# Performance work log

Measured on AMD Instinct MI355X. Metric: run time of the kernel, lower is better.

Reference implementation:

```python
import jax, jax.numpy as jnp
import numpy as np

HIDDEN = 64
IN_SIZE = 2048 + 512  # sum(obs_shape) + sum(action_shape)


def setup_inputs() -> dict:
    key = jax.random.key(0)
    ks = jax.random.split(key, 10)
    B = 32768
    s_in = 1.0 / np.sqrt(IN_SIZE)
    s_h = 1.0 / np.sqrt(HIDDEN)
    return {
        "state": jax.random.normal(ks[0], (B, 2048), dtype=jnp.float32),
        "action": jax.random.normal(ks[1], (B, 512), dtype=jnp.float32),
        "hidden_state": jax.random.normal(ks[2], (B, HIDDEN), dtype=jnp.float32),
        "cell_state": jax.random.normal(ks[3], (B, HIDDEN), dtype=jnp.float32),
        # fused gate weights, gate order: [i, f, g, o]
        "Wi": jax.random.uniform(ks[4], (IN_SIZE, 4 * HIDDEN), jnp.float32, -s_in, s_in),
        "bi": jax.random.uniform(ks[5], (4 * HIDDEN,), jnp.float32, -s_in, s_in),
        "Wh": jax.random.uniform(ks[6], (HIDDEN, 4 * HIDDEN), jnp.float32, -s_h, s_h),
        "bh": jax.random.uniform(ks[7], (4 * HIDDEN,), jnp.float32, -s_h, s_h),
        "Wo": jax.random.uniform(ks[8], (HIDDEN, 1), jnp.float32, -s_h, s_h),
        "bo": jax.random.uniform(ks[9], (1,), jnp.float32, -s_h, s_h),
    }


def reference(state, action, hidden_state, cell_state, Wi, bi, Wh, bh, Wo, bo):
    x = jnp.concatenate([state, action], axis=1)  # [B, IN_SIZE]
    # two fused GEMMs covering all 8 Linear layers (gate order i,f,g,o)
    gates = x @ Wi + bi + hidden_state @ Wh + bh  # [B, 4*HIDDEN]
    i_t, f_t, g_t, o_t = jnp.split(gates, 4, axis=1)
    i_t = jax.nn.sigmoid(i_t)
    f_t = jax.nn.sigmoid(f_t)
    g_t = jnp.tanh(g_t)
    o_t = jax.nn.sigmoid(o_t)
    c_t = f_t * cell_state + i_t * g_t
    h_t = o_t * jnp.tanh(c_t)
    out = jnp.tanh(h_t @ Wo + bo)  # [B, 1]
    return (out, h_t, c_t)
```

## Files before the change

### kernel.cpp

```cpp
#include <hip/hip_runtime.h>
#include <hip/hip_bf16.h>

#define K_IN 2624
#define NSTEP 82
#define NCHUNK 82

typedef __attribute__((ext_vector_type(8))) short short8;
typedef __attribute__((ext_vector_type(4))) float float4_t;

__device__ __forceinline__ short f2bf(float f) {
    union { __hip_bfloat16 b; short s; } u;
    u.b = __float2bfloat16(f);
    return u.s;
}

__device__ __forceinline__ float sigmoid_fast(float x) {
    return 1.f / (1.f + __expf(-x));
}

__device__ __forceinline__ float tanh_fast(float x) {
    float e = __expf(-2.f * fabsf(x));
    float t = (1.f - e) / (1.f + e);
    return copysignf(t, x);
}

__device__ __forceinline__ void async16(const void* g, void* l) {
    __builtin_amdgcn_global_load_lds(
        (__attribute__((address_space(1))) void*)g,
        (__attribute__((address_space(3))) void*)l, 16, 0, 0);
}

__global__ void prep_kernel(const float* __restrict__ Wi, const float* __restrict__ bi,
                            const float* __restrict__ Wh, const float* __restrict__ bh,
                            short* __restrict__ Wt2, float* __restrict__ bsum) {
    __shared__ short tile[32][264];
    const int t = threadIdx.x;
    const int kb = blockIdx.x;
    const int k0 = kb * 32;

#pragma unroll 8
    for (int j = 0; j < 32; ++j) {
        int k = k0 + j;
        float v = (k < 2560) ? Wi[(size_t)k * 256 + t]
                             : Wh[(size_t)(k - 2560) * 256 + t];
        tile[j][t] = f2bf(v);
    }
    if (kb == 0) bsum[t] = bi[t] + bh[t];
    __syncthreads();

#pragma unroll
    for (int c = 0; c < 4; ++c) {
        int idx = c * 256 + t;
        int lane = idx & 63;
        int nb = idx >> 6;
        int n = nb * 16 + (lane & 15);
        int j0 = (lane >> 4) * 8;
        short8 v;
#pragma unroll
        for (int j = 0; j < 8; ++j) v[j] = tile[j0 + j][n];
        *reinterpret_cast<short8*>(Wt2 + (size_t)kb * 8192 + (size_t)idx * 8) = v;
    }
}

__global__ __launch_bounds__(256, 2)
void lstm_kernel(const float* __restrict__ state, const float* __restrict__ action,
                 const float* __restrict__ hidden, const float* __restrict__ cell,
                 const short* __restrict__ Wt2, const float* __restrict__ bsum,
                 const float* __restrict__ Wo, const float* __restrict__ bo,
                 float* __restrict__ out, int Brows) {
    __shared__ __align__(16) char smem[49152];
    char* const sA = smem;
    char* const sB = smem + 16384;

    const int t = threadIdx.x;
    const int w = t >> 6;
    const int l = t & 63;
    const int lr = l & 15;
    const int q = l >> 4;
    const int bm = blockIdx.x;

    const int rsub = l >> 3;
    const int scol = (l & 7) ^ rsub;
    const char* aSrc[2];
    auto setA = [&](const float* p, int strideF) {
#pragma unroll
        for (int i = 0; i < 2; ++i) {
            size_t grow = (size_t)bm * 64 + w * 16 + i * 8 + rsub;
            aSrc[i] = (const char*)(p + grow * (size_t)strideF) + scol * 16;
        }
    };

    auto issueAB = [&](int buf, const char* bS) {
#pragma unroll
        for (int j = 0; j < 4; ++j)
            async16(bS + j * 1024, sB + buf * 16384 + (w * 4 + j) * 1024);
#pragma unroll
        for (int i = 0; i < 2; ++i) {
            async16(aSrc[i], sA + buf * 8192 + (w * 16 + i * 8) * 128);
            aSrc[i] += 128;
        }
    };

    float4_t acc[16];
#pragma unroll
    for (int nb = 0; nb < 16; ++nb) acc[nb] = (float4_t)(bsum[nb * 16 + lr]);

    setA(state, 2048);
    const char* bS0 = (const char*)Wt2 + (w * 4) * 1024 + l * 16;
    issueAB(0, bS0);
    issueAB(1, bS0 + 16384);
    const char* bSn = bS0 + 2 * 16384;

    const char* const sAb = sA + (w * 16 + lr) * 128;
    const char* const sBb = sB + l * 16;
    const int g0 = (2 * q) ^ (lr & 7);
    const int g1 = (2 * q + 1) ^ (lr & 7);

    auto compute = [&](int buf) {
        const char* bufA = sAb + buf * 8192;
        const char* bufB = sBb + buf * 16384;
        float4_t lo = *(const float4_t*)(bufA + g0 * 16);
        float4_t hi = *(const float4_t*)(bufA + g1 * 16);
        short8 a;
        a[0] = f2bf(lo[0]); a[1] = f2bf(lo[1]); a[2] = f2bf(lo[2]); a[3] = f2bf(lo[3]);
        a[4] = f2bf(hi[0]); a[5] = f2bf(hi[1]); a[6] = f2bf(hi[2]); a[7] = f2bf(hi[3]);
#pragma unroll
        for (int nb = 0; nb < 16; ++nb) {
            short8 b = *(const short8*)(bufB + nb * 1024);
            acc[nb] = __builtin_amdgcn_mfma_f32_16x16x32_bf16(a, b, acc[nb], 0, 0, 0);
        }
    };

    for (int k = 0; k < NCHUNK - 1; ++k) {
        asm volatile("s_waitcnt vmcnt(6)" ::: "memory");
        __builtin_amdgcn_s_barrier();
        asm volatile("" ::: "memory");
        compute(k & 1);
        asm volatile("" ::: "memory");
        __builtin_amdgcn_s_barrier();
        asm volatile("" ::: "memory");
        const int kk = k + 2;
        if (kk < NCHUNK) {
            if (kk == 64) setA(action, 512);
            if (kk == 80) setA(hidden, 64);
            issueAB(k & 1, bSn);
            bSn += 16384;
        }
    }
    asm volatile("s_waitcnt vmcnt(0)" ::: "memory");
    __builtin_amdgcn_s_barrier();
    asm volatile("" ::: "memory");
    compute((NCHUNK - 1) & 1);

    const float bov = bo[0];
    float wo_[4];
#pragma unroll
    for (int nb0 = 0; nb0 < 4; ++nb0) wo_[nb0] = Wo[nb0 * 16 + lr];

    const size_t rowbase = (size_t)bm * 64 + w * 16 + q * 4;
    float* outH = out + Brows;
    float* outC = outH + (size_t)Brows * 64;

#pragma unroll
    for (int r = 0; r < 4; ++r) {
        const size_t grow = rowbase + r;
        float vpart = 0.f;
#pragma unroll
        for (int nb0 = 0; nb0 < 4; ++nb0) {
            const int n = nb0 * 16 + lr;
            const float i_t = sigmoid_fast(acc[nb0][r]);
            const float f_t = sigmoid_fast(acc[nb0 + 4][r]);
            const float g_t = tanh_fast(acc[nb0 + 8][r]);
            const float o_t = sigmoid_fast(acc[nb0 + 12][r]);
            const float c_t = f_t * cell[grow * 64 + n] + i_t * g_t;
            const float h_t = o_t * tanh_fast(c_t);
            outC[grow * 64 + n] = c_t;
            outH[grow * 64 + n] = h_t;
            vpart += h_t * wo_[nb0];
        }
        vpart += __shfl_xor(vpart, 1);
        vpart += __shfl_xor(vpart, 2);
        vpart += __shfl_xor(vpart, 4);
        vpart += __shfl_xor(vpart, 8);
        if (lr == 0) out[grow] = tanh_fast(vpart + bov);
    }
}

extern "C" void kernel_launch(void* const* d_in, const int* in_sizes, int n_in,
                              void* d_out, int out_size, void* d_ws, size_t ws_size,
                              hipStream_t stream) {
    const float* state  = (const float*)d_in[0];
    const float* action = (const float*)d_in[1];
    const float* hidden = (const float*)d_in[2];
    const float* cell   = (const float*)d_in[3];
    const float* Wi     = (const float*)d_in[4];
    const float* bi     = (const float*)d_in[5];
    const float* Wh     = (const float*)d_in[6];
    const float* bh     = (const float*)d_in[7];
    const float* Wo     = (const float*)d_in[8];
    const float* bo     = (const float*)d_in[9];

    const int Brows = in_sizes[0] / 2048;

    short* Wt2  = (short*)d_ws;
    float* bsum = (float*)((char*)d_ws + (size_t)NSTEP * 8192 * sizeof(short));

    prep_kernel<<<NSTEP, 256, 0, stream>>>(Wi, bi, Wh, bh, Wt2, bsum);
    lstm_kernel<<<Brows / 64, 256, 0, stream>>>(state, action, hidden, cell,
                                                Wt2, bsum, Wo, bo, (float*)d_out, Brows);
}
```

Baseline: 447.9 us.

## Retile LSTM GEMM so each wave owns gate columns across all rows, triple-buffer

Each wave now computes a 64x64 tile (all 64 rows, one 16-column slice of each of the four gates) instead of 16 rows by 256 columns. This cuts the per-wave B-fragment LDS reads from 16 to 4 per k-step at the cost of four A-fragment loads and conversions. The loads move to a three-stage LDS ring with one barrier per iteration (LDS grows to 72KB) and MFMA issue priority is raised. The final output reduction now goes through shared memory across waves. The larger LDS footprint may prevent two blocks from sharing a CU, lowering occupancy.

```diff
diff --git a/kernel.cpp b/kernel.cpp
--- a/kernel.cpp
+++ b/kernel.cpp
@@ -68,9 +68,9 @@
                  const short* __restrict__ Wt2, const float* __restrict__ bsum,
                  const float* __restrict__ Wo, const float* __restrict__ bo,
                  float* __restrict__ out, int Brows) {
-    __shared__ __align__(16) char smem[49152];
-    char* const sA = smem;
-    char* const sB = smem + 16384;
+    __shared__ __align__(16) char smem[73728];
+    char* const sB = smem;
+    char* const sA = smem + 49152;
 
     const int t = threadIdx.x;
     const int w = t >> 6;
@@ -101,88 +101,106 @@
         }
     };
 
-    float4_t acc[16];
-#pragma unroll
-    for (int nb = 0; nb < 16; ++nb) acc[nb] = (float4_t)(bsum[nb * 16 + lr]);
+    float4_t acc[4][4];
+#pragma unroll
+    for (int m = 0; m < 4; ++m)
+#pragma unroll
+        for (int j = 0; j < 4; ++j)
+            acc[m][j] = (float4_t)(bsum[(w + 4 * j) * 16 + lr]);
 
     setA(state, 2048);
-    const char* bS0 = (const char*)Wt2 + (w * 4) * 1024 + l * 16;
-    issueAB(0, bS0);
-    issueAB(1, bS0 + 16384);
-    const char* bSn = bS0 + 2 * 16384;
-
-    const char* const sAb = sA + (w * 16 + lr) * 128;
-    const char* const sBb = sB + l * 16;
+    const char* bSn = (const char*)Wt2 + (w * 4) * 1024 + l * 16;
+    issueAB(0, bSn); bSn += 16384;
+    issueAB(1, bSn); bSn += 16384;
+
+    const char* const sAb = sA + lr * 128;
+    const char* const sBb = sB + w * 1024 + l * 16;
     const int g0 = (2 * q) ^ (lr & 7);
-    const int g1 = (2 * q + 1) ^ (lr & 7);
+    const int g1 = g0 ^ 1;
 
     auto compute = [&](int buf) {
         const char* bufA = sAb + buf * 8192;
         const char* bufB = sBb + buf * 16384;
-        float4_t lo = *(const float4_t*)(bufA + g0 * 16);
-        float4_t hi = *(const float4_t*)(bufA + g1 * 16);
-        short8 a;
-        a[0] = f2bf(lo[0]); a[1] = f2bf(lo[1]); a[2] = f2bf(lo[2]); a[3] = f2bf(lo[3]);
-        a[4] = f2bf(hi[0]); a[5] = f2bf(hi[1]); a[6] = f2bf(hi[2]); a[7] = f2bf(hi[3]);
-#pragma unroll
-        for (int nb = 0; nb < 16; ++nb) {
-            short8 b = *(const short8*)(bufB + nb * 1024);
-            acc[nb] = __builtin_amdgcn_mfma_f32_16x16x32_bf16(a, b, acc[nb], 0, 0, 0);
-        }
+        short8 b[4], a[4];
+#pragma unroll
+        for (int j = 0; j < 4; ++j)
+            b[j] = *(const short8*)(bufB + j * 4096);
+#pragma unroll
+        for (int m = 0; m < 4; ++m) {
+            float4_t lo = *(const float4_t*)(bufA + m * 2048 + g0 * 16);
+            float4_t hi = *(const float4_t*)(bufA + m * 2048 + g1 * 16);
+            short8 av;
+            av[0] = f2bf(lo[0]); av[1] = f2bf(lo[1]); av[2] = f2bf(lo[2]); av[3] = f2bf(lo[3]);
+            av[4] = f2bf(hi[0]); av[5] = f2bf(hi[1]); av[6] = f2bf(hi[2]); av[7] = f2bf(hi[3]);
+            a[m] = av;
+        }
+        __builtin_amdgcn_s_setprio(1);
+#pragma unroll
+        for (int m = 0; m < 4; ++m)
+#pragma unroll
+            for (int j = 0; j < 4; ++j)
+                acc[m][j] = __builtin_amdgcn_mfma_f32_16x16x32_bf16(a[m], b[j], acc[m][j], 0, 0, 0);
+        __builtin_amdgcn_s_setprio(0);
     };
 
+    int cb = 0, ib = 2;
     for (int k = 0; k < NCHUNK - 1; ++k) {
         asm volatile("s_waitcnt vmcnt(6)" ::: "memory");
-        __builtin_amdgcn_s_barrier();
-        asm volatile("" ::: "memory");
-        compute(k & 1);
-        asm volatile("" ::: "memory");
         __builtin_amdgcn_s_barrier();
         asm volatile("" ::: "memory");
         const int kk = k + 2;
         if (kk < NCHUNK) {
             if (kk == 64) setA(action, 512);
             if (kk == 80) setA(hidden, 64);
-            issueAB(k & 1, bSn);
+            issueAB(ib, bSn);
             bSn += 16384;
-        }
+            ib = (ib == 2) ? 0 : ib + 1;
+        }
+        compute(cb);
+        cb = (cb == 2) ? 0 : cb + 1;
     }
     asm volatile("s_waitcnt vmcnt(0)" ::: "memory");
     __builtin_amdgcn_s_barrier();
     asm volatile("" ::: "memory");
-    compute((NCHUNK - 1) & 1);
+    compute(cb);
 
     const float bov = bo[0];
-    float wo_[4];
-#pragma unroll
-    for (int nb0 = 0; nb0 < 4; ++nb0) wo_[nb0] = Wo[nb0 * 16 + lr];
-
-    const size_t rowbase = (size_t)bm * 64 + w * 16 + q * 4;
+    const float wo = Wo[w * 16 + lr];
+    const int n0 = w * 16 + lr;
     float* outH = out + Brows;
     float* outC = outH + (size_t)Brows * 64;
-
-#pragma unroll
-    for (int r = 0; r < 4; ++r) {
-        const size_t grow = rowbase + r;
-        float vpart = 0.f;
-#pragma unroll
-        for (int nb0 = 0; nb0 < 4; ++nb0) {
-            const int n = nb0 * 16 + lr;
-            const float i_t = sigmoid_fast(acc[nb0][r]);
-            const float f_t = sigmoid_fast(acc[nb0 + 4][r]);
-            const float g_t = tanh_fast(acc[nb0 + 8][r]);
-            const float o_t = sigmoid_fast(acc[nb0 + 12][r]);
-            const float c_t = f_t * cell[grow * 64 + n] + i_t * g_t;
-            const float h_t = o_t * tanh_fast(c_t);
-            outC[grow * 64 + n] = c_t;
-            outH[grow * 64 + n] = h_t;
-            vpart += h_t * wo_[nb0];
-        }
-        vpart += __shfl_xor(vpart, 1);
-        vpart += __shfl_xor(vpart, 2);
-        vpart += __shfl_xor(vpart, 4);
-        vpart += __shfl_xor(vpart, 8);
-        if (lr == 0) out[grow] = tanh_fast(vpart + bov);
+    float* sPart = (float*)smem;
+
+    __builtin_amdgcn_s_barrier();
+    asm volatile("" ::: "memory");
+
+#pragma unroll
+    for (int m = 0; m < 4; ++m) {
+#pragma unroll
+        for (int r = 0; r < 4; ++r) {
+            const int row = m * 16 + q * 4 + r;
+            const size_t grow = (size_t)bm * 64 + row;
+            float i_t = sigmoid_fast(acc[m][0][r]);
+            float f_t = sigmoid_fast(acc[m][1][r]);
+            float g_t = tanh_fast(acc[m][2][r]);
+            float o_t = sigmoid_fast(acc[m][3][r]);
+            float c_t = f_t * cell[grow * 64 + n0] + i_t * g_t;
+            float h_t = o_t * tanh_fast(c_t);
+            outC[grow * 64 + n0] = c_t;
+            outH[grow * 64 + n0] = h_t;
+            float v = h_t * wo;
+            v += __shfl_xor(v, 1);
+            v += __shfl_xor(v, 2);
+            v += __shfl_xor(v, 4);
+            v += __shfl_xor(v, 8);
+            if (lr == 0) sPart[row * 4 + w] = v;
+        }
+    }
+    __syncthreads();
+    if (t < 64) {
+        float s = sPart[t * 4 + 0] + sPart[t * 4 + 1]
+                + sPart[t * 4 + 2] + sPart[t * 4 + 3];
+        out[(size_t)bm * 64 + t] = tanh_fast(s + bov);
     }
 }
 
```

After: 448.7 us. Within noise of the previous version (+0.2%).
